# Performance work log

Measured on AMD Instinct MI355X. Metric: run time of the kernel, lower is better.

## Reference

```python
import jax, jax.numpy as jnp
import numpy as np

B, S, D = 8, 2048, 256


def setup_inputs() -> dict:
    key = jax.random.key(0)
    kq, kk, kv, km = jax.random.split(key, 4)
    q = jax.random.normal(kq, (B, S, D), dtype=jnp.float32)
    k = jax.random.normal(kk, (B, S, D), dtype=jnp.float32)
    v = jax.random.normal(kv, (B, S, D), dtype=jnp.float32)
    mask = jax.random.randint(km, (B, S, S), 0, 2, dtype=jnp.int32)
    return {"q": q, "k": k, "v": v, "mask": mask}


def reference(q, k, v, mask):
    d_k = q.shape[-1]
    scale = 1.0 / jnp.sqrt(jnp.float32(d_k))
    # scores: [B, S, S]
    attn = jnp.einsum('bqd,bkd->bqk', q, k) * scale
    attn = jnp.where(mask == 0, jnp.float32(-1e9), attn)
    attn = jax.nn.softmax(attn, axis=-1)
    out = jnp.einsum('bqk,bkd->bqd', attn, v)
    return (out, attn)
```

## Files before the change

kernel.cpp:

```cpp
#include <hip/hip_runtime.h>

constexpr int B = 8, S = 2048, D = 256;
constexpr int TQ = 32;
constexpr float SCALE = 0.0625f;
constexpr int PSTRIDE = 2056;

typedef __attribute__((ext_vector_type(8))) short bf16x8;
typedef __attribute__((ext_vector_type(4))) float f32x4;

__device__ __forceinline__ short f2bf(float f) {
    union { float f; unsigned u; } c; c.f = f;
    unsigned u = c.u + 0x7fffu + ((c.u >> 16) & 1u);
    return (short)(u >> 16);
}

__global__ __launch_bounds__(256) void prepass(
    const float* __restrict__ k, const float* __restrict__ v,
    short* __restrict__ kb, short* __restrict__ vtb)
{
    __shared__ float tile[64][65];
    const int blk = blockIdx.x;
    const int tid = threadIdx.x;

    if (blk < 4096) {
        int i = blk * 256 + tid;
        float4 x = ((const float4*)k)[i];
        short4 o; o.x = f2bf(x.x); o.y = f2bf(x.y); o.z = f2bf(x.z); o.w = f2bf(x.w);
        ((short4*)kb)[i] = o;
    } else {
        int blk2 = blk - 4096;
        int b = blk2 >> 7, rem = blk2 & 127;
        int d0 = (rem & 3) * 64, k0 = (rem >> 2) * 64;
        int tr = tid >> 4, tc = tid & 15;
        const float* vb = v + (size_t)b * S * D;
        #pragma unroll
        for (int r = 0; r < 4; ++r) {
            int key = r * 16 + tr;
            float4 x = *(const float4*)(vb + (size_t)(k0 + key) * D + d0 + tc * 4);
            tile[key][tc * 4 + 0] = x.x; tile[key][tc * 4 + 1] = x.y;
            tile[key][tc * 4 + 2] = x.z; tile[key][tc * 4 + 3] = x.w;
        }
        __syncthreads();
        short* vtbb = vtb + (size_t)b * D * S;
        #pragma unroll
        for (int r = 0; r < 4; ++r) {
            int d = r * 16 + tr;
            short4 o;
            o.x = f2bf(tile[tc * 4 + 0][d]); o.y = f2bf(tile[tc * 4 + 1][d]);
            o.z = f2bf(tile[tc * 4 + 2][d]); o.w = f2bf(tile[tc * 4 + 3][d]);
            *(short4*)(vtbb + (size_t)(d0 + d) * S + k0 + tc * 4) = o;
        }
    }
}

__global__ __launch_bounds__(512, 2) void attn_mfma(
    const float* __restrict__ qf, const short* __restrict__ kb,
    const short* __restrict__ vtb, const int* __restrict__ maskg,
    float* __restrict__ outg, float* __restrict__ attng)
{
    const int b = blockIdx.x & 7;
    const int i0 = (blockIdx.x >> 3) * TQ;
    const int tid = threadIdx.x;
    const int wave = tid >> 6, lane = tid & 63;
    const int quad = lane >> 4, l16 = lane & 15;

    __shared__ short p_lds[TQ][PSTRIDE];
    __shared__ float red[8][TQ];
    __shared__ unsigned short pm_lds[TQ][8][16];

    {
        const int* mrow_base = maskg + ((size_t)b * S + i0 + wave * 4) * S;
        #pragma unroll 1
        for (int rr = 0; rr < 4; ++rr) {
            const int* mrow = mrow_base + (size_t)rr * S;
            int mv[32];
            #pragma unroll
            for (int g = 0; g < 8; ++g)
                #pragma unroll
                for (int u = 0; u < 4; ++u)
                    mv[g * 4 + u] = mrow[g * 256 + u * 64 + lane];
            #pragma unroll
            for (int g = 0; g < 8; ++g) {
                unsigned v16 = 0;
                #pragma unroll
                for (int u = 0; u < 4; ++u) {
                    unsigned long long bal = __ballot(mv[g * 4 + u] != 0);
                    unsigned nib = (unsigned)((bal >> l16) & 1ull)
                                 | (unsigned)((bal >> (l16 + 16)) & 1ull) << 1
                                 | (unsigned)((bal >> (l16 + 32)) & 1ull) << 2
                                 | (unsigned)((bal >> (l16 + 48)) & 1ull) << 3;
                    v16 |= nib << (u * 4);
                }
                if (lane < 16) pm_lds[wave * 4 + rr][g][l16] = (unsigned short)v16;
            }
        }
    }
    __syncthreads();

    bf16x8 aq[2][8];
    const float* qbase = qf + ((size_t)b * S + i0) * D;
    #pragma unroll
    for (int mt = 0; mt < 2; ++mt)
        #pragma unroll
        for (int ks = 0; ks < 8; ++ks) {
            const float* p = qbase + (size_t)(mt * 16 + l16) * D + ks * 32 + quad * 8;
            float4 x0 = *(const float4*)p;
            float4 x1 = *(const float4*)(p + 4);
            bf16x8 a;
            a[0] = f2bf(x0.x); a[1] = f2bf(x0.y); a[2] = f2bf(x0.z); a[3] = f2bf(x0.w);
            a[4] = f2bf(x1.x); a[5] = f2bf(x1.y); a[6] = f2bf(x1.z); a[7] = f2bf(x1.w);
            aq[mt][ks] = a;
        }

    f32x4 acc[2][16];
    #pragma unroll
    for (int mt = 0; mt < 2; ++mt)
        #pragma unroll
        for (int nt = 0; nt < 16; ++nt)
            acc[mt][nt] = f32x4{0.f, 0.f, 0.f, 0.f};

    const short* kbase = kb + (size_t)b * S * D;
    #pragma unroll
    for (int nt = 0; nt < 16; ++nt) {
        const int n0 = wave * 256 + nt * 16;
        bf16x8 bk[8];
        #pragma unroll
        for (int ks = 0; ks < 8; ++ks)
            bk[ks] = *(const bf16x8*)(kbase + (size_t)(n0 + l16) * D + ks * 32 + quad * 8);
        #pragma unroll
        for (int ks = 0; ks < 8; ++ks) {
            acc[0][nt] = __builtin_amdgcn_mfma_f32_16x16x32_bf16(aq[0][ks], bk[ks], acc[0][nt], 0, 0, 0);
            acc[1][nt] = __builtin_amdgcn_mfma_f32_16x16x32_bf16(aq[1][ks], bk[ks], acc[1][nt], 0, 0, 0);
        }
    }

    unsigned pmv[2][4];
    #pragma unroll
    for (int mt = 0; mt < 2; ++mt)
        #pragma unroll
        for (int r = 0; r < 4; ++r)
            pmv[mt][r] = pm_lds[mt * 16 + quad * 4 + r][wave][l16];

    float rsum[2][4];
    #pragma unroll
    for (int mt = 0; mt < 2; ++mt)
        #pragma unroll
        for (int r = 0; r < 4; ++r) rsum[mt][r] = 0.f;

    #pragma unroll
    for (int mt = 0; mt < 2; ++mt) {
        #pragma unroll
        for (int nt = 0; nt < 16; ++nt) {
            #pragma unroll
            for (int r = 0; r < 4; ++r) {
                float s = acc[mt][nt][r] * SCALE;
                float sv = ((pmv[mt][r] >> nt) & 1u) ? s : -1e9f;
                float e = __expf(sv);
                acc[mt][nt][r] = e;
                rsum[mt][r] += e;
            }
        }
    }
    #pragma unroll
    for (int mt = 0; mt < 2; ++mt)
        #pragma unroll
        for (int r = 0; r < 4; ++r) {
            float v = rsum[mt][r];
            v += __shfl_xor(v, 1); v += __shfl_xor(v, 2);
            v += __shfl_xor(v, 4); v += __shfl_xor(v, 8);
            rsum[mt][r] = v;
            if (l16 == 0) red[wave][mt * 16 + quad * 4 + r] = v;
        }
    __syncthreads();

    float inv[2][4];
    #pragma unroll
    for (int mt = 0; mt < 2; ++mt)
        #pragma unroll
        for (int r = 0; r < 4; ++r) {
            float tot = 0.f;
            #pragma unroll
            for (int w = 0; w < 8; ++w) tot += red[w][mt * 16 + quad * 4 + r];
            inv[mt][r] = 1.0f / tot;
        }

    #pragma unroll
    for (int mt = 0; mt < 2; ++mt) {
        float* abase = attng + ((size_t)b * S + i0 + mt * 16 + quad * 4) * S;
        #pragma unroll
        for (int nt = 0; nt < 16; ++nt) {
            const int col = wave * 256 + nt * 16 + l16;
            #pragma unroll
            for (int r = 0; r < 4; ++r) {
                float p = acc[mt][nt][r] * inv[mt][r];
                abase[(size_t)r * S + col] = p;
                p_lds[mt * 16 + quad * 4 + r][col] = f2bf(p);
            }
        }
    }
    __syncthreads();

    f32x4 oacc[2][2];
    #pragma unroll
    for (int mt = 0; mt < 2; ++mt)
        #pragma unroll
        for (int nc = 0; nc < 2; ++nc) oacc[mt][nc] = f32x4{0.f, 0.f, 0.f, 0.f};

    const short* vbase = vtb + (size_t)b * D * S;
    const int nb = wave * 32;
    for (int ks = 0; ks < 64; ++ks) {
        bf16x8 ap[2], bv[2];
        #pragma unroll
        for (int mt = 0; mt < 2; ++mt)
            ap[mt] = *(const bf16x8*)&p_lds[mt * 16 + l16][ks * 32 + quad * 8];
        #pragma unroll
        for (int nc = 0; nc < 2; ++nc)
            bv[nc] = *(const bf16x8*)(vbase + (size_t)(nb + nc * 16 + l16) * S + ks * 32 + quad * 8);
        #pragma unroll
        for (int mt = 0; mt < 2; ++mt)
            #pragma unroll
            for (int nc = 0; nc < 2; ++nc)
                oacc[mt][nc] = __builtin_amdgcn_mfma_f32_16x16x32_bf16(ap[mt], bv[nc], oacc[mt][nc], 0, 0, 0);
    }

    #pragma unroll
    for (int mt = 0; mt < 2; ++mt)
        #pragma unroll
        for (int nc = 0; nc < 2; ++nc)
            #pragma unroll
            for (int r = 0; r < 4; ++r) {
                int row = i0 + mt * 16 + quad * 4 + r;
                int col = nb + nc * 16 + l16;
                outg[((size_t)b * S + row) * D + col] = oacc[mt][nc][r];
            }
}

extern "C" void kernel_launch(void* const* d_in, const int* in_sizes, int n_in,
                              void* d_out, int out_size, void* d_ws, size_t ws_size,
                              hipStream_t stream) {
    const float* q    = (const float*)d_in[0];
    const float* k    = (const float*)d_in[1];
    const float* v    = (const float*)d_in[2];
    const int*   mask = (const int*)d_in[3];
    float* out  = (float*)d_out;
    float* attn = out + (size_t)B * S * D;

    const size_t N = (size_t)B * S * D;
    short* kb  = (short*)d_ws;
    short* vtb = kb + N;

    prepass<<<dim3(5120), 256, 0, stream>>>(k, v, kb, vtb);
    attn_mfma<<<dim3((S / TQ) * B), 512, 0, stream>>>(q, kb, vtb, mask, out, attn);
}
```

Baseline: 411.0 us.

## Transpose score MFMA so each lane owns contiguous columns; vectorize mask and attn I/O

Swaps the MFMA operand order so the score accumulator is transposed. Each lane then holds four consecutive key columns of one query row. This lets the mask load directly as int4 into a per-lane 64-bit bitmask, dropping the ballot/LDS prepass and its barrier. It also lets the attention output be written as float4 and the bf16 probabilities as short4, replacing scalar strided stores. Masked entries become exact zeros instead of exp(-1e9), and the row-sum reduction shuffles across quads instead of within a 16-lane group.

```diff
diff --git a/kernel.cpp b/kernel.cpp
--- a/kernel.cpp
+++ b/kernel.cpp
@@ -66,36 +66,30 @@
 
     __shared__ short p_lds[TQ][PSTRIDE];
     __shared__ float red[8][TQ];
-    __shared__ unsigned short pm_lds[TQ][8][16];
-
-    {
-        const int* mrow_base = maskg + ((size_t)b * S + i0 + wave * 4) * S;
-        #pragma unroll 1
-        for (int rr = 0; rr < 4; ++rr) {
-            const int* mrow = mrow_base + (size_t)rr * S;
-            int mv[32];
-            #pragma unroll
-            for (int g = 0; g < 8; ++g)
-                #pragma unroll
-                for (int u = 0; u < 4; ++u)
-                    mv[g * 4 + u] = mrow[g * 256 + u * 64 + lane];
-            #pragma unroll
-            for (int g = 0; g < 8; ++g) {
-                unsigned v16 = 0;
-                #pragma unroll
-                for (int u = 0; u < 4; ++u) {
-                    unsigned long long bal = __ballot(mv[g * 4 + u] != 0);
-                    unsigned nib = (unsigned)((bal >> l16) & 1ull)
-                                 | (unsigned)((bal >> (l16 + 16)) & 1ull) << 1
-                                 | (unsigned)((bal >> (l16 + 32)) & 1ull) << 2
-                                 | (unsigned)((bal >> (l16 + 48)) & 1ull) << 3;
-                    v16 |= nib << (u * 4);
-                }
-                if (lane < 16) pm_lds[wave * 4 + rr][g][l16] = (unsigned short)v16;
+
+    unsigned long long mb[2];
+    #pragma unroll
+    for (int mt = 0; mt < 2; ++mt) {
+        const int* mrow = maskg + ((size_t)b * S + i0 + mt * 16 + l16) * S + wave * 256 + quad * 4;
+        unsigned long long bits = 0;
+        #pragma unroll
+        for (int c = 0; c < 2; ++c) {
+            int4 t[8];
+            #pragma unroll
+            for (int j = 0; j < 8; ++j)
+                t[j] = *(const int4*)(mrow + (c * 8 + j) * 16);
+            #pragma unroll
+            for (int j = 0; j < 8; ++j) {
+                const int nt = c * 8 + j;
+                unsigned long long nib = (t[j].x != 0 ? 1ull : 0ull)
+                                       | (t[j].y != 0 ? 2ull : 0ull)
+                                       | (t[j].z != 0 ? 4ull : 0ull)
+                                       | (t[j].w != 0 ? 8ull : 0ull);
+                bits |= nib << (nt * 4);
             }
         }
-    }
-    __syncthreads();
+        mb[mt] = bits;
+    }
 
     bf16x8 aq[2][8];
     const float* qbase = qf + ((size_t)b * S + i0) * D;
@@ -129,73 +123,56 @@
             bk[ks] = *(const bf16x8*)(kbase + (size_t)(n0 + l16) * D + ks * 32 + quad * 8);
         #pragma unroll
         for (int ks = 0; ks < 8; ++ks) {
-            acc[0][nt] = __builtin_amdgcn_mfma_f32_16x16x32_bf16(aq[0][ks], bk[ks], acc[0][nt], 0, 0, 0);
-            acc[1][nt] = __builtin_amdgcn_mfma_f32_16x16x32_bf16(aq[1][ks], bk[ks], acc[1][nt], 0, 0, 0);
-        }
-    }
-
-    unsigned pmv[2][4];
-    #pragma unroll
-    for (int mt = 0; mt < 2; ++mt)
-        #pragma unroll
-        for (int r = 0; r < 4; ++r)
-            pmv[mt][r] = pm_lds[mt * 16 + quad * 4 + r][wave][l16];
-
-    float rsum[2][4];
-    #pragma unroll
-    for (int mt = 0; mt < 2; ++mt)
-        #pragma unroll
-        for (int r = 0; r < 4; ++r) rsum[mt][r] = 0.f;
-
+            acc[0][nt] = __builtin_amdgcn_mfma_f32_16x16x32_bf16(bk[ks], aq[0][ks], acc[0][nt], 0, 0, 0);
+            acc[1][nt] = __builtin_amdgcn_mfma_f32_16x16x32_bf16(bk[ks], aq[1][ks], acc[1][nt], 0, 0, 0);
+        }
+    }
+
+    float rsum[2] = {0.f, 0.f};
     #pragma unroll
     for (int mt = 0; mt < 2; ++mt) {
         #pragma unroll
         for (int nt = 0; nt < 16; ++nt) {
             #pragma unroll
             for (int r = 0; r < 4; ++r) {
-                float s = acc[mt][nt][r] * SCALE;
-                float sv = ((pmv[mt][r] >> nt) & 1u) ? s : -1e9f;
-                float e = __expf(sv);
+                float e = ((mb[mt] >> (nt * 4 + r)) & 1ull)
+                        ? __expf(acc[mt][nt][r] * SCALE) : 0.0f;
                 acc[mt][nt][r] = e;
-                rsum[mt][r] += e;
+                rsum[mt] += e;
             }
         }
     }
     #pragma unroll
-    for (int mt = 0; mt < 2; ++mt)
-        #pragma unroll
-        for (int r = 0; r < 4; ++r) {
-            float v = rsum[mt][r];
-            v += __shfl_xor(v, 1); v += __shfl_xor(v, 2);
-            v += __shfl_xor(v, 4); v += __shfl_xor(v, 8);
-            rsum[mt][r] = v;
-            if (l16 == 0) red[wave][mt * 16 + quad * 4 + r] = v;
-        }
+    for (int mt = 0; mt < 2; ++mt) {
+        float v = rsum[mt];
+        v += __shfl_xor(v, 16); v += __shfl_xor(v, 32);
+        if (quad == 0) red[wave][mt * 16 + l16] = v;
+    }
     __syncthreads();
 
-    float inv[2][4];
-    #pragma unroll
-    for (int mt = 0; mt < 2; ++mt)
-        #pragma unroll
-        for (int r = 0; r < 4; ++r) {
-            float tot = 0.f;
-            #pragma unroll
-            for (int w = 0; w < 8; ++w) tot += red[w][mt * 16 + quad * 4 + r];
-            inv[mt][r] = 1.0f / tot;
-        }
-
-    #pragma unroll
-    for (int mt = 0; mt < 2; ++mt) {
-        float* abase = attng + ((size_t)b * S + i0 + mt * 16 + quad * 4) * S;
+    float inv[2];
+    #pragma unroll
+    for (int mt = 0; mt < 2; ++mt) {
+        float tot = 0.f;
+        #pragma unroll
+        for (int w = 0; w < 8; ++w) tot += red[w][mt * 16 + l16];
+        inv[mt] = 1.0f / tot;
+    }
+
+    #pragma unroll
+    for (int mt = 0; mt < 2; ++mt) {
+        float* arow = attng + ((size_t)b * S + i0 + mt * 16 + l16) * S + wave * 256 + quad * 4;
         #pragma unroll
         for (int nt = 0; nt < 16; ++nt) {
-            const int col = wave * 256 + nt * 16 + l16;
-            #pragma unroll
-            for (int r = 0; r < 4; ++r) {
-                float p = acc[mt][nt][r] * inv[mt][r];
-                abase[(size_t)r * S + col] = p;
-                p_lds[mt * 16 + quad * 4 + r][col] = f2bf(p);
-            }
+            float4 p4; short4 pb;
+            float p0 = acc[mt][nt][0] * inv[mt];
+            float p1 = acc[mt][nt][1] * inv[mt];
+            float p2 = acc[mt][nt][2] * inv[mt];
+            float p3 = acc[mt][nt][3] * inv[mt];
+            p4.x = p0; p4.y = p1; p4.z = p2; p4.w = p3;
+            pb.x = f2bf(p0); pb.y = f2bf(p1); pb.z = f2bf(p2); pb.w = f2bf(p3);
+            *(float4*)(arow + nt * 16) = p4;
+            *(short4*)&p_lds[mt * 16 + l16][wave * 256 + nt * 16 + quad * 4] = pb;
         }
     }
     __syncthreads();
```

Result: no change. 409.5 us (-0.4%).
